# Optimization experiments

Hardware: AMD Instinct MI355X
Metric: run time of the kernel (lower is better)

Reference implementation:

```python
import jax, jax.numpy as jnp
import numpy as np

RADIUS = 3  # local window half-size -> K = (2*RADIUS+1)**2 = 49 taps


def _bilinear_sample_zeros(img_flat, x, y, h, w):
    """Bilinear sampling with zeros padding (grid_sample, align_corners=True).
    img_flat: (B, C, H*W); x, y: (P, K) pixel-space coords. Returns (B, C, P, K).
    align_corners=True denormalization exactly inverts the normalization in the
    original module, so we sample directly at pixel coordinates.
    """
    B, C, _ = img_flat.shape
    x0 = jnp.floor(x)
    y0 = jnp.floor(y)
    out = jnp.zeros((B, C) + x.shape, dtype=img_flat.dtype)
    corners = [
        (x0,       y0,       (x0 + 1 - x) * (y0 + 1 - y)),
        (x0 + 1.0, y0,       (x - x0) * (y0 + 1 - y)),
        (x0,       y0 + 1.0, (x0 + 1 - x) * (y - y0)),
        (x0 + 1.0, y0 + 1.0, (x - x0) * (y - y0)),
    ]
    for xi, yi, wt in corners:
        inb = (xi >= 0) & (xi < w) & (yi >= 0) & (yi < h)
        xi_c = jnp.clip(xi, 0, w - 1).astype(jnp.int32)
        yi_c = jnp.clip(yi, 0, h - 1).astype(jnp.int32)
        idx = (yi_c * w + xi_c).reshape(-1)            # (P*K,)
        v = jnp.take(img_flat, idx, axis=2)            # (B, C, P*K)
        v = v.reshape(B, C, *x.shape)                  # (B, C, P, K)
        out = out + v * (wt * inb.astype(img_flat.dtype))[None, None]
    return out


def reference(feature0, feature1):
    n, c, s, h, w = feature0.shape
    B = n * s
    f0 = feature0.transpose(0, 2, 1, 3, 4).reshape(B, c, h, w)
    f1 = feature1.transpose(0, 2, 1, 3, 4).reshape(B, c, h, w)

    r = RADIUS
    # base pixel coords (x, y), flattened row-major over (h, w) -> (P, 2)
    yy, xx = jnp.meshgrid(jnp.arange(h, dtype=jnp.float32),
                          jnp.arange(w, dtype=jnp.float32), indexing='ij')
    base = jnp.stack([xx, yy], axis=-1).reshape(h * w, 2)  # (P, 2)

    # window offsets (dx, dy), dy outer / dx inner ordering -> (K, 2)
    dys, dxs = jnp.meshgrid(jnp.arange(-r, r + 1, dtype=jnp.float32),
                            jnp.arange(-r, r + 1, dtype=jnp.float32), indexing='ij')
    offs = jnp.stack([dxs, dys], axis=-1).reshape(-1, 2)   # (K, 2)

    sample = base[:, None, :] + offs[None, :, :]           # (P, K, 2)
    valid = ((sample[..., 0] >= 0) & (sample[..., 0] < w) &
             (sample[..., 1] >= 0) & (sample[..., 1] < h))  # (P, K)

    f1_flat = f1.reshape(B, c, h * w)
    wf = _bilinear_sample_zeros(f1_flat, sample[..., 0], sample[..., 1], h, w)  # (B, c, P, K)

    f0_flat = f0.reshape(B, c, h * w)
    corr = jnp.einsum('bcp,bcpk->bpk', f0_flat, wf) / jnp.asarray(c, jnp.float32) ** 0.5
    corr = jnp.where(valid[None], corr, -jnp.inf)
    prob = jax.nn.softmax(corr, axis=-1)                   # (B, P, K)

    corresp = jnp.einsum('bpk,pkj->bpj', prob, sample)     # (B, P, 2) expected (x, y)
    flow = corresp - base[None]                            # (B, P, 2)
    flow = flow.reshape(n, s, h, w, 2).transpose(0, 4, 1, 2, 3)  # (n, 2, s, h, w)
    return flow


def setup_inputs() -> dict:
    key = jax.random.key(0)
    k0, k1 = jax.random.split(key)
    n, c, s, h, w = 2, 64, 4, 64, 44
    feature0 = jax.random.normal(k0, (n, c, s, h, w), dtype=jnp.float32)
    feature1 = jax.random.normal(k1, (n, c, s, h, w), dtype=jnp.float32)
    return {"feature0": feature0, "feature1": feature1}
```

## Files before the change

### kernel.cpp

```cpp
#include <hip/hip_runtime.h>
#include <math.h>

#define N_  2
#define C_  64
#define S_  4
#define H_  64
#define W_  44
#define HW_       (H_ * W_)
#define CH_STRIDE (S_ * HW_)
#define NSTRIDE   (C_ * S_ * HW_)

typedef _Float16 h2 __attribute__((ext_vector_type(2)));
typedef _Float16 h8 __attribute__((ext_vector_type(8)));

#if defined(__has_builtin)
#  if __has_builtin(__builtin_amdgcn_fdot2)
#    define FDOT2(a, b, c) __builtin_amdgcn_fdot2((a), (b), (c), false)
#  endif
#endif
#ifndef FDOT2
#  define FDOT2(a, b, c) ((float)(a).x * (float)(b).x + (float)(a).y * (float)(b).y + (c))
#endif

__global__ __launch_bounds__(448) void flow_kernel(
    const float* __restrict__ f0,
    const float* __restrict__ f1,
    float* __restrict__ out)
{
    const int lane = threadIdx.x & 63;
    const int wid  = threadIdx.x >> 6;

    const int b = blockIdx.x & 7;
    const int y = blockIdx.x >> 3;
    const int n_idx = b >> 2;
    const int s_idx = b & 3;
    const int base  = n_idx * NSTRIDE + s_idx * HW_;

    __shared__ __align__(16) char lds_raw[7 * 8 * W_ * 8 * 2];
    _Float16* lds_h = (_Float16*)lds_raw;

    const int x   = lane;
    const int xe  = min(x, W_ - 1);
    const int row = y + wid - 3;
    const bool row_ok = (row >= 0) && (row < H_);

    float acc[7] = {0.f, 0.f, 0.f, 0.f, 0.f, 0.f, 0.f};

    _Float16* slab = lds_h + wid * (8 * W_ * 8);

    if (row_ok) {
        const float* f1p = f1 + base + row * W_ + xe;
        #pragma unroll 2
        for (int c8 = 0; c8 < 8; ++c8) {
            const float* cp1 = f1p + (size_t)(c8 * 8) * CH_STRIDE;
            float v[8];
            #pragma unroll
            for (int j = 0; j < 8; ++j) v[j] = cp1[(size_t)j * CH_STRIDE];
            h8 pk;
            #pragma unroll
            for (int j = 0; j < 8; ++j) pk[j] = (_Float16)v[j];
            if (x < W_)
                *(h8*)&slab[(c8 * W_ + x) * 8] = pk;
        }

        const float* f0p = f0 + base + y * W_ + xe;
        int xt[7];
        #pragma unroll
        for (int dx = 0; dx < 7; ++dx)
            xt[dx] = min(max(x + dx - 3, 0), W_ - 1);

        #pragma unroll 2
        for (int c8 = 0; c8 < 8; ++c8) {
            const float* cp0 = f0p + (size_t)(c8 * 8) * CH_STRIDE;
            float a[8];
            #pragma unroll
            for (int j = 0; j < 8; ++j) a[j] = cp0[(size_t)j * CH_STRIDE];
            h2 a2[4];
            #pragma unroll
            for (int j = 0; j < 4; ++j) {
                h2 t; t.x = (_Float16)a[2 * j]; t.y = (_Float16)a[2 * j + 1];
                a2[j] = t;
            }
            const _Float16* rp = &slab[c8 * W_ * 8];
            #pragma unroll
            for (int dx = 0; dx < 7; ++dx) {
                const h8 t = *(const h8*)&rp[xt[dx] * 8];
                h2 t01, t23, t45, t67;
                t01.x = t[0]; t01.y = t[1];
                t23.x = t[2]; t23.y = t[3];
                t45.x = t[4]; t45.y = t[5];
                t67.x = t[6]; t67.y = t[7];
                float s = acc[dx];
                s = FDOT2(a2[0], t01, s);
                s = FDOT2(a2[1], t23, s);
                s = FDOT2(a2[2], t45, s);
                s = FDOT2(a2[3], t67, s);
                acc[dx] = s;
            }
        }
    }

    __syncthreads();

    float (*corr)[49] = (float(*)[49])lds_raw;
    if (x < W_) {
        #pragma unroll
        for (int dx = 0; dx < 7; ++dx)
            corr[x][wid * 7 + dx] = acc[dx] * 0.125f;
    }

    __syncthreads();

    if (wid == 0) {
        float c[49];
        float m = -1e30f;
        #pragma unroll
        for (int k = 0; k < 49; ++k) {
            const int dy  = k / 7, dx = k % 7;
            const int col = x + dx - 3;
            const int rr  = y + dy - 3;
            const bool ok = (col >= 0) && (col < W_) && (rr >= 0) && (rr < H_);
            const float v = ok ? corr[xe][k] : -1e30f;
            c[k] = v;
            m = fmaxf(m, v);
        }
        float S = 0.0f, Sx = 0.0f, Sy = 0.0f;
        #pragma unroll
        for (int k = 0; k < 49; ++k) {
            const float e = __expf(c[k] - m);
            S  += e;
            Sx += e * (float)(k % 7 - 3);
            Sy += e * (float)(k / 7 - 3);
        }
        if (lane < W_) {
            const float inv = 1.0f / S;
            const int ob = (n_idx * 2) * S_ * HW_ + s_idx * HW_ + y * W_ + lane;
            out[ob]            = Sx * inv;
            out[ob + S_ * HW_] = Sy * inv;
        }
    }
}

extern "C" void kernel_launch(void* const* d_in, const int* in_sizes, int n_in,
                              void* d_out, int out_size, void* d_ws, size_t ws_size,
                              hipStream_t stream) {
    const float* f0 = (const float*)d_in[0];
    const float* f1 = (const float*)d_in[1];
    float* out = (float*)d_out;

    flow_kernel<<<8 * H_, 448, 0, stream>>>(f0, f1, out);
}
```

Baseline: 67.30 us.

## Split channel reduction across two wave halves with batched loads

Doubles the block to 14 waves, with each pair of waves splitting the 64 channels into two halves of 32. Each wave issues all 32 f1 and 32 f0 loads up front before a block barrier, then computes partial 7-tap correlations. The two halves are combined through a separate LDS corr buffer with an extra barrier. The aim is more memory-level parallelism and more waves to hide global load latency. The cost is higher register pressure (64 floats held live) and an extra synchronisation plus a read-modify-write pass through LDS.

```diff
diff --git a/kernel.cpp b/kernel.cpp
--- a/kernel.cpp
+++ b/kernel.cpp
@@ -22,13 +22,15 @@
 #  define FDOT2(a, b, c) ((float)(a).x * (float)(b).x + (float)(a).y * (float)(b).y + (c))
 #endif
 
-__global__ __launch_bounds__(448) void flow_kernel(
+__global__ __launch_bounds__(896) void flow_kernel(
     const float* __restrict__ f0,
     const float* __restrict__ f1,
     float* __restrict__ out)
 {
     const int lane = threadIdx.x & 63;
-    const int wid  = threadIdx.x >> 6;
+    const int w    = threadIdx.x >> 6;
+    const int dy   = (w < 7) ? w : (w - 7);
+    const int half = (w < 7) ? 0 : 1;
 
     const int b = blockIdx.x & 7;
     const int y = blockIdx.x >> 3;
@@ -36,52 +38,60 @@
     const int s_idx = b & 3;
     const int base  = n_idx * NSTRIDE + s_idx * HW_;
 
-    __shared__ __align__(16) char lds_raw[7 * 8 * W_ * 8 * 2];
+    __shared__ __align__(16) char lds_raw[7 * 5632 + W_ * 49 * 4];
     _Float16* lds_h = (_Float16*)lds_raw;
+    float (*corr)[49] = (float(*)[49])(lds_raw + 7 * 5632);
 
     const int x   = lane;
     const int xe  = min(x, W_ - 1);
-    const int row = y + wid - 3;
+    const int row = y + dy - 3;
     const bool row_ok = (row >= 0) && (row < H_);
 
     float acc[7] = {0.f, 0.f, 0.f, 0.f, 0.f, 0.f, 0.f};
 
-    _Float16* slab = lds_h + wid * (8 * W_ * 8);
+    _Float16* slab = lds_h + dy * 2816;
+    const int ch0 = half * 32;
+
+    float a[32];
 
     if (row_ok) {
-        const float* f1p = f1 + base + row * W_ + xe;
-        #pragma unroll 2
-        for (int c8 = 0; c8 < 8; ++c8) {
-            const float* cp1 = f1p + (size_t)(c8 * 8) * CH_STRIDE;
-            float v[8];
+        const float* f1p = f1 + base + row * W_ + xe + (size_t)ch0 * CH_STRIDE;
+        float v[32];
+        #pragma unroll
+        for (int j = 0; j < 32; ++j) v[j] = f1p[(size_t)j * CH_STRIDE];
+
+        const float* f0p = f0 + base + y * W_ + xe + (size_t)ch0 * CH_STRIDE;
+        #pragma unroll
+        for (int j = 0; j < 32; ++j) a[j] = f0p[(size_t)j * CH_STRIDE];
+
+        if (x < W_) {
             #pragma unroll
-            for (int j = 0; j < 8; ++j) v[j] = cp1[(size_t)j * CH_STRIDE];
-            h8 pk;
-            #pragma unroll
-            for (int j = 0; j < 8; ++j) pk[j] = (_Float16)v[j];
-            if (x < W_)
-                *(h8*)&slab[(c8 * W_ + x) * 8] = pk;
+            for (int c8l = 0; c8l < 4; ++c8l) {
+                h8 pk;
+                #pragma unroll
+                for (int j = 0; j < 8; ++j) pk[j] = (_Float16)v[c8l * 8 + j];
+                *(h8*)&slab[((4 * half + c8l) * W_ + x) * 8] = pk;
+            }
         }
+    }
 
-        const float* f0p = f0 + base + y * W_ + xe;
+    __syncthreads();
+
+    if (row_ok) {
+        h2 a2[16];
+        #pragma unroll
+        for (int j = 0; j < 16; ++j) {
+            h2 t; t.x = (_Float16)a[2 * j]; t.y = (_Float16)a[2 * j + 1];
+            a2[j] = t;
+        }
         int xt[7];
         #pragma unroll
         for (int dx = 0; dx < 7; ++dx)
             xt[dx] = min(max(x + dx - 3, 0), W_ - 1);
 
-        #pragma unroll 2
-        for (int c8 = 0; c8 < 8; ++c8) {
-            const float* cp0 = f0p + (size_t)(c8 * 8) * CH_STRIDE;
-            float a[8];
-            #pragma unroll
-            for (int j = 0; j < 8; ++j) a[j] = cp0[(size_t)j * CH_STRIDE];
-            h2 a2[4];
-            #pragma unroll
-            for (int j = 0; j < 4; ++j) {
-                h2 t; t.x = (_Float16)a[2 * j]; t.y = (_Float16)a[2 * j + 1];
-                a2[j] = t;
-            }
-            const _Float16* rp = &slab[c8 * W_ * 8];
+        #pragma unroll
+        for (int c8l = 0; c8l < 4; ++c8l) {
+            const _Float16* rp = &slab[(4 * half + c8l) * W_ * 8];
             #pragma unroll
             for (int dx = 0; dx < 7; ++dx) {
                 const h8 t = *(const h8*)&rp[xt[dx] * 8];
@@ -91,34 +101,36 @@
                 t45.x = t[4]; t45.y = t[5];
                 t67.x = t[6]; t67.y = t[7];
                 float s = acc[dx];
-                s = FDOT2(a2[0], t01, s);
-                s = FDOT2(a2[1], t23, s);
-                s = FDOT2(a2[2], t45, s);
-                s = FDOT2(a2[3], t67, s);
+                s = FDOT2(a2[c8l * 4 + 0], t01, s);
+                s = FDOT2(a2[c8l * 4 + 1], t23, s);
+                s = FDOT2(a2[c8l * 4 + 2], t45, s);
+                s = FDOT2(a2[c8l * 4 + 3], t67, s);
                 acc[dx] = s;
             }
         }
     }
 
+    if (half == 0 && row_ok && x < W_) {
+        #pragma unroll
+        for (int dx = 0; dx < 7; ++dx)
+            corr[x][dy * 7 + dx] = acc[dx] * 0.125f;
+    }
+    __syncthreads();
+    if (half == 1 && row_ok && x < W_) {
+        #pragma unroll
+        for (int dx = 0; dx < 7; ++dx)
+            corr[x][dy * 7 + dx] += acc[dx] * 0.125f;
+    }
     __syncthreads();
 
-    float (*corr)[49] = (float(*)[49])lds_raw;
-    if (x < W_) {
-        #pragma unroll
-        for (int dx = 0; dx < 7; ++dx)
-            corr[x][wid * 7 + dx] = acc[dx] * 0.125f;
-    }
-
-    __syncthreads();
-
-    if (wid == 0) {
+    if (w == 0) {
         float c[49];
         float m = -1e30f;
         #pragma unroll
         for (int k = 0; k < 49; ++k) {
-            const int dy  = k / 7, dx = k % 7;
-            const int col = x + dx - 3;
-            const int rr  = y + dy - 3;
+            const int kdy = k / 7, kdx = k % 7;
+            const int col = x + kdx - 3;
+            const int rr  = y + kdy - 3;
             const bool ok = (col >= 0) && (col < W_) && (rr >= 0) && (rr < H_);
             const float v = ok ? corr[xe][k] : -1e30f;
             c[k] = v;
@@ -148,5 +160,5 @@
     const float* f1 = (const float*)d_in[1];
     float* out = (float*)d_out;
 
-    flow_kernel<<<8 * H_, 448, 0, stream>>>(f0, f1, out);
+    flow_kernel<<<8 * H_, 896, 0, stream>>>(f0, f1, out);
 }
```

Result: slower. 70.05 us (+4.1%).

## Stage f0 row in LDS via eighth wave and batch all 64 channel loads

Applied to the files above, without the earlier changes.

Adds an eighth wavefront that stages the f0 row into LDS as fp16 alongside the seven f1 rows. The seven compute waves then read f0 from shared memory instead of each reloading it from global memory. Each staging thread now issues all 64 strided channel loads up front so more memory requests are in flight. The corr buffer gets its own LDS array, which removes one barrier but raises LDS use and register pressure from the 64-element array.

```diff
diff --git a/kernel.cpp b/kernel.cpp
--- a/kernel.cpp
+++ b/kernel.cpp
@@ -22,13 +22,13 @@
 #  define FDOT2(a, b, c) ((float)(a).x * (float)(b).x + (float)(a).y * (float)(b).y + (c))
 #endif
 
-__global__ __launch_bounds__(448) void flow_kernel(
+__global__ __launch_bounds__(512) void flow_kernel(
     const float* __restrict__ f0,
     const float* __restrict__ f1,
     float* __restrict__ out)
 {
     const int lane = threadIdx.x & 63;
-    const int wid  = threadIdx.x >> 6;
+    const int w    = threadIdx.x >> 6;
 
     const int b = blockIdx.x & 7;
     const int y = blockIdx.x >> 3;
@@ -36,52 +36,55 @@
     const int s_idx = b & 3;
     const int base  = n_idx * NSTRIDE + s_idx * HW_;
 
-    __shared__ __align__(16) char lds_raw[7 * 8 * W_ * 8 * 2];
-    _Float16* lds_h = (_Float16*)lds_raw;
+    __shared__ __align__(16) _Float16 slabs[8 * 8 * W_ * 8];
+    __shared__ float corr[W_][49];
 
-    const int x   = lane;
-    const int xe  = min(x, W_ - 1);
-    const int row = y + wid - 3;
-    const bool row_ok = (row >= 0) && (row < H_);
+    const int x  = lane;
+    const int xe = min(x, W_ - 1);
 
-    float acc[7] = {0.f, 0.f, 0.f, 0.f, 0.f, 0.f, 0.f};
+    const int  r      = (w == 7) ? y : (y + w - 3);
+    const bool stg_ok = (r >= 0) && (r < H_);
+    const float* src  = (w == 7) ? f0 : f1;
 
-    _Float16* slab = lds_h + wid * (8 * W_ * 8);
+    if (stg_ok) {
+        const float* p = src + base + r * W_ + xe;
+        float v[64];
+        #pragma unroll
+        for (int j = 0; j < 64; ++j)
+            v[j] = p[(size_t)j * CH_STRIDE];
+        if (x < W_) {
+            #pragma unroll
+            for (int c8 = 0; c8 < 8; ++c8) {
+                h8 pk;
+                #pragma unroll
+                for (int j = 0; j < 8; ++j) pk[j] = (_Float16)v[c8 * 8 + j];
+                *(h8*)&slabs[((w * 8 + c8) * W_ + x) * 8] = pk;
+            }
+        }
+    }
 
-    if (row_ok) {
-        const float* f1p = f1 + base + row * W_ + xe;
-        #pragma unroll 2
-        for (int c8 = 0; c8 < 8; ++c8) {
-            const float* cp1 = f1p + (size_t)(c8 * 8) * CH_STRIDE;
-            float v[8];
-            #pragma unroll
-            for (int j = 0; j < 8; ++j) v[j] = cp1[(size_t)j * CH_STRIDE];
-            h8 pk;
-            #pragma unroll
-            for (int j = 0; j < 8; ++j) pk[j] = (_Float16)v[j];
-            if (x < W_)
-                *(h8*)&slab[(c8 * W_ + x) * 8] = pk;
-        }
+    __syncthreads();
 
-        const float* f0p = f0 + base + y * W_ + xe;
+    if (w < 7 && stg_ok) {
+        float acc[7] = {0.f, 0.f, 0.f, 0.f, 0.f, 0.f, 0.f};
         int xt[7];
         #pragma unroll
         for (int dx = 0; dx < 7; ++dx)
             xt[dx] = min(max(x + dx - 3, 0), W_ - 1);
 
-        #pragma unroll 2
+        const _Float16* f0slab = &slabs[(7 * 8) * W_ * 8];
+        const _Float16* myslab = &slabs[(w * 8) * W_ * 8];
+
+        #pragma unroll
         for (int c8 = 0; c8 < 8; ++c8) {
-            const float* cp0 = f0p + (size_t)(c8 * 8) * CH_STRIDE;
-            float a[8];
-            #pragma unroll
-            for (int j = 0; j < 8; ++j) a[j] = cp0[(size_t)j * CH_STRIDE];
+            const h8 af = *(const h8*)&f0slab[(c8 * W_ + xe) * 8];
             h2 a2[4];
             #pragma unroll
             for (int j = 0; j < 4; ++j) {
-                h2 t; t.x = (_Float16)a[2 * j]; t.y = (_Float16)a[2 * j + 1];
+                h2 t; t.x = af[2 * j]; t.y = af[2 * j + 1];
                 a2[j] = t;
             }
-            const _Float16* rp = &slab[c8 * W_ * 8];
+            const _Float16* rp = &myslab[c8 * W_ * 8];
             #pragma unroll
             for (int dx = 0; dx < 7; ++dx) {
                 const h8 t = *(const h8*)&rp[xt[dx] * 8];
@@ -98,27 +101,24 @@
                 acc[dx] = s;
             }
         }
+
+        if (x < W_) {
+            #pragma unroll
+            for (int dx = 0; dx < 7; ++dx)
+                corr[x][w * 7 + dx] = acc[dx] * 0.125f;
+        }
     }
 
     __syncthreads();
 
-    float (*corr)[49] = (float(*)[49])lds_raw;
-    if (x < W_) {
-        #pragma unroll
-        for (int dx = 0; dx < 7; ++dx)
-            corr[x][wid * 7 + dx] = acc[dx] * 0.125f;
-    }
-
-    __syncthreads();
-
-    if (wid == 0) {
+    if (w == 0) {
         float c[49];
         float m = -1e30f;
         #pragma unroll
         for (int k = 0; k < 49; ++k) {
-            const int dy  = k / 7, dx = k % 7;
-            const int col = x + dx - 3;
-            const int rr  = y + dy - 3;
+            const int kdy = k / 7, kdx = k % 7;
+            const int col = x + kdx - 3;
+            const int rr  = y + kdy - 3;
             const bool ok = (col >= 0) && (col < W_) && (rr >= 0) && (rr < H_);
             const float v = ok ? corr[xe][k] : -1e30f;
             c[k] = v;
@@ -148,5 +148,5 @@
     const float* f1 = (const float*)d_in[1];
     float* out = (float*)d_out;
 
-    flow_kernel<<<8 * H_, 448, 0, stream>>>(f0, f1, out);
+    flow_kernel<<<8 * H_, 512, 0, stream>>>(f0, f1, out);
 }
```

New measurement: 66.22 us. No clear change (-1.6%).
